# Kernel tuning notes

Measured on AMD Instinct MI355X. Metric: run time of the kernel, lower is better.

The kernel has to match this reference:

```python
import jax, jax.numpy as jnp
import numpy as np

NUM_TIMES = 1024  # times are drawn from [0, 1024), used as fixed segment count
N = 16777216


def setup_inputs() -> dict:
    key = jax.random.key(0)
    k1, k2, k3 = jax.random.split(key, 3)
    outs = jax.random.normal(k1, (N,), dtype=jnp.float32)
    T_E = jax.random.randint(k2, (N,), 0, 2, dtype=jnp.int32)
    T_T = jax.random.randint(k3, (N,), 0, NUM_TIMES, dtype=jnp.int32)
    return {"outs": outs, "T_E": T_E, "T_T": T_T}


def reference(outs, T_E, T_T):
    # E[E > 0] = 1  -> binary event indicator
    E = (T_E > 0).astype(outs.dtype)
    # Y_label_T = |T_T| ; integer times act directly as segment ids
    seg_ids = jnp.abs(T_T)
    Obs = jnp.sum(E)
    # log of running sum of hazards: log(cumsum(exp(yhat)))
    y_hat_cumsum = jnp.log(jnp.cumsum(jnp.exp(outs)))
    # original segment_max initializes accumulator at 0, so it is clipped below at 0;
    # jnp.maximum also neutralizes -inf fill for empty segments (count=0 there anyway)
    seg_max = jnp.maximum(
        jax.ops.segment_max(y_hat_cumsum, seg_ids, num_segments=NUM_TIMES), 0.0
    )
    seg_cnt = jax.ops.segment_sum(E, seg_ids, num_segments=NUM_TIMES)
    loss_s2 = jnp.sum(seg_max * seg_cnt)
    loss_s1 = jnp.sum(outs * E)
    return (loss_s2 - loss_s1) / Obs
```

## Files before the change

kernel.cpp:

```cpp
#include <hip/hip_runtime.h>

#define NUM_SEGS 1024
#define CHUNK_LOG 13
#define CHUNK (1 << CHUNK_LOG)
#define SUBCH 4
#define SUPER (CHUNK * SUBCH)
#define BLK 512
#define NWAVE (BLK / 64)
#define SEGBLK 256

__device__ __forceinline__ float waveReduceSumF(float v) {
#pragma unroll
    for (int off = 32; off > 0; off >>= 1) v += __shfl_down(v, off, 64);
    return v;
}
__device__ __forceinline__ double waveReduceSumD(double v) {
#pragma unroll
    for (int off = 32; off > 0; off >>= 1) v += __shfl_down(v, off, 64);
    return v;
}
__device__ __forceinline__ unsigned waveReduceSumU(unsigned v) {
#pragma unroll
    for (int off = 32; off > 0; off >>= 1) v += __shfl_down(v, off, 64);
    return v;
}
__device__ __forceinline__ int waveReduceMaxI(int v) {
#pragma unroll
    for (int off = 32; off > 0; off >>= 1) {
        const int o = __shfl_down(v, off, 64);
        v = o > v ? o : v;
    }
    return v;
}

__global__ void init_kernel(unsigned* __restrict__ seg_cnt,
                            float* __restrict__ csums, int nChunks,
                            unsigned* __restrict__ obs,
                            double* __restrict__ loss1,
                            double* __restrict__ loss2,
                            unsigned* __restrict__ done) {
    const int t = blockIdx.x * blockDim.x + threadIdx.x;
    if (t < NUM_SEGS) seg_cnt[t] = 0u;
    if (t < nChunks) csums[t] = 0.f;
    if (t == 0) { obs[0] = 0u; loss1[0] = 0.0; loss2[0] = 0.0; done[0] = 0u; }
}

__global__ __launch_bounds__(BLK, 4) void pass1_kernel(
    const float* __restrict__ outs, const int* __restrict__ te,
    const int* __restrict__ tt, int N, int nChunks,
    float* __restrict__ csums, unsigned* __restrict__ seg_cnt,
    unsigned* __restrict__ obs, double* __restrict__ loss1) {
    __shared__ unsigned hist[NUM_SEGS];
    __shared__ float redF[NWAVE];
    __shared__ unsigned redU[NWAVE];

    for (int t = threadIdx.x; t < NUM_SEGS; t += BLK) hist[t] = 0u;
    __syncthreads();

    const int lane = threadIdx.x & 63;
    const int wid = threadIdx.x >> 6;
    const int superBase = blockIdx.x * SUPER;

    float sE[SUBCH] = {0.f, 0.f, 0.f, 0.f};
    float sumOE = 0.f;
    unsigned cntE = 0u;

    if (superBase + SUPER <= N) {
#pragma unroll
        for (int u = 0; u < SUBCH * 4; ++u) {
            const int k = u >> 2, it = u & 3;
            const int i = superBase + (k << CHUNK_LOG) + (wid << 10) + (it << 8) +
                          (lane << 2);
            const float4 o = *reinterpret_cast<const float4*>(outs + i);
            const int4 ev = *reinterpret_cast<const int4*>(te + i);
            const int4 sv = *reinterpret_cast<const int4*>(tt + i);
            const float e0 = __expf(o.x), e1 = __expf(o.y);
            const float e2 = __expf(o.z), e3 = __expf(o.w);
            sE[k] += (e0 + e1) + (e2 + e3);
            const int s0 = sv.x < 0 ? -sv.x : sv.x;
            const int s1 = sv.y < 0 ? -sv.y : sv.y;
            const int s2 = sv.z < 0 ? -sv.z : sv.z;
            const int s3 = sv.w < 0 ? -sv.w : sv.w;
            if (ev.x > 0) { cntE++; sumOE += o.x; atomicAdd(&hist[s0], 1u); }
            if (ev.y > 0) { cntE++; sumOE += o.y; atomicAdd(&hist[s1], 1u); }
            if (ev.z > 0) { cntE++; sumOE += o.z; atomicAdd(&hist[s2], 1u); }
            if (ev.w > 0) { cntE++; sumOE += o.w; atomicAdd(&hist[s3], 1u); }
        }
    } else {
        for (int k = 0; k < SUBCH; ++k) {
            const int cbase = superBase + k * CHUNK;
            if (cbase >= N) break;
            const int end = (cbase + CHUNK < N) ? cbase + CHUNK : N;
            for (int i = cbase + (int)threadIdx.x; i < end; i += BLK) {
                const float o = outs[i];
                const int e = te[i];
                int s = tt[i]; s = s < 0 ? -s : s;
                sE[k] += __expf(o);
                if (e > 0) { cntE++; sumOE += o; atomicAdd(&hist[s], 1u); }
            }
        }
    }

#pragma unroll
    for (int k = 0; k < SUBCH; ++k) {
        const float w = waveReduceSumF(sE[k]);
        if (lane == 0) {
            const int cidx = (superBase >> CHUNK_LOG) + k;
            if (cidx < nChunks) atomicAdd(&csums[cidx], w);
        }
    }

    __syncthreads();

    for (int t = threadIdx.x; t < NUM_SEGS; t += BLK) {
        const unsigned h = hist[t];
        if (h) atomicAdd(&seg_cnt[t], h);
    }

    const float wOE = waveReduceSumF(sumOE);
    const unsigned wC = waveReduceSumU(cntE);
    if (lane == 0) { redF[wid] = wOE; redU[wid] = wC; }
    __syncthreads();
    if (threadIdx.x == 0) {
        float oe = 0.f; unsigned c = 0u;
#pragma unroll
        for (int j = 0; j < NWAVE; ++j) { oe += redF[j]; c += redU[j]; }
        atomicAdd(loss1, (double)oe);
        atomicAdd(obs, c);
    }
}

__global__ __launch_bounds__(SEGBLK) void seg_final_kernel(
    const float* __restrict__ outs, const int* __restrict__ tt,
    const float* __restrict__ csums, const unsigned* __restrict__ seg_cnt,
    const double* __restrict__ loss1, double* __restrict__ loss2,
    const unsigned* __restrict__ obs, unsigned* __restrict__ done,
    float* __restrict__ out, int N, int nChunks) {
    __shared__ double redD[SEGBLK / 64];
    __shared__ float redF[SEGBLK / 64];
    __shared__ int redI[SEGBLK / 64];
    __shared__ int s_li;

    const int t = blockIdx.x;
    const unsigned cnt = seg_cnt[t];
    const int lane = threadIdx.x & 63, wid = threadIdx.x >> 6;

    if (cnt != 0u) {
        int c = nChunks - 1;
        int LI = -1;
        for (;;) {
            const int base = c << CHUNK_LOG;
            const int end = (base + CHUNK < N) ? base + CHUNK : N;
            const int span = end - base;
            const int qspan = span & ~3;
            int li = -1;
            for (int i = base + ((int)threadIdx.x << 2); i < base + qspan;
                 i += SEGBLK * 4) {
                const int4 sv = *reinterpret_cast<const int4*>(tt + i);
                const int s0 = sv.x < 0 ? -sv.x : sv.x;
                const int s1 = sv.y < 0 ? -sv.y : sv.y;
                const int s2 = sv.z < 0 ? -sv.z : sv.z;
                const int s3 = sv.w < 0 ? -sv.w : sv.w;
                if (s3 == t) li = i + 3;
                else if (s2 == t) li = i + 2;
                else if (s1 == t) li = i + 1;
                else if (s0 == t) li = i;
            }
            for (int i = base + qspan + (int)threadIdx.x; i < end; i += SEGBLK) {
                int s = tt[i]; s = s < 0 ? -s : s;
                if (s == t && i > li) li = i;
            }
            li = waveReduceMaxI(li);
            if (lane == 0) redI[wid] = li;
            __syncthreads();
            if (threadIdx.x == 0) {
                int m = redI[0];
#pragma unroll
                for (int j = 1; j < SEGBLK / 64; ++j) m = redI[j] > m ? redI[j] : m;
                s_li = m;
            }
            __syncthreads();
            LI = s_li;
            if (LI >= 0 || --c < 0) break;
        }

        if (LI >= 0) {
            double p = 0.0;
            for (int j = threadIdx.x; j < c; j += SEGBLK) p += (double)csums[j];
            p = waveReduceSumD(p);
            if (lane == 0) redD[wid] = p;

            const int base = c << CHUNK_LOG;
            float fs = 0.f;
            for (int i = base + (int)threadIdx.x; i <= LI; i += SEGBLK)
                fs += __expf(outs[i]);
            fs = waveReduceSumF(fs);
            if (lane == 0) redF[wid] = fs;
            __syncthreads();
            if (threadIdx.x == 0) {
                double pre = 0.0;
                float fsum = 0.f;
#pragma unroll
                for (int j = 0; j < SEGBLK / 64; ++j) { pre += redD[j]; fsum += redF[j]; }
                double sm = log(pre + (double)fsum);
                if (sm < 0.0) sm = 0.0;
                atomicAdd(loss2, sm * (double)cnt);
            }
        }
    }

    if (threadIdx.x == 0) {
        __threadfence();
        const unsigned d = atomicAdd(done, 1u);
        if (d == (unsigned)(gridDim.x - 1)) {
            const double l2 = atomicAdd(loss2, 0.0);
            const double l1 = *(volatile const double*)loss1;
            const unsigned o = *(volatile const unsigned*)obs;
            out[0] = (float)((l2 - l1) / (double)o);
        }
    }
}

extern "C" void kernel_launch(void* const* d_in, const int* in_sizes, int n_in,
                              void* d_out, int out_size, void* d_ws, size_t ws_size,
                              hipStream_t stream) {
    const float* outs = (const float*)d_in[0];
    const int* te = (const int*)d_in[1];
    const int* tt = (const int*)d_in[2];
    const int N = in_sizes[0];
    float* out = (float*)d_out;

    const int nChunks = (N + CHUNK - 1) / CHUNK;

    char* ws = (char*)d_ws;
    double* d_loss1 = (double*)ws;
    double* d_loss2 = d_loss1 + 1;
    float* d_csums = (float*)(ws + 16);
    unsigned* d_segcnt = (unsigned*)(d_csums + nChunks);
    unsigned* d_obs = d_segcnt + NUM_SEGS;
    unsigned* d_done = d_obs + 1;

    const int initThreads = (nChunks > NUM_SEGS ? nChunks : NUM_SEGS);
    init_kernel<<<(initThreads + 255) / 256, 256, 0, stream>>>(
        d_segcnt, d_csums, nChunks, d_obs, d_loss1, d_loss2, d_done);
    const int nSuper = (N + SUPER - 1) / SUPER;
    pass1_kernel<<<nSuper, BLK, 0, stream>>>(outs, te, tt, N, nChunks, d_csums,
                                             d_segcnt, d_obs, d_loss1);
    seg_final_kernel<<<NUM_SEGS, SEGBLK, 0, stream>>>(
        outs, tt, d_csums, d_segcnt, d_loss1, d_loss2, d_obs, d_done, out, N,
        nChunks);
}
```

Baseline: 249.2 us.

## Batch deeper loads per thread and reduce chunk sums in shared memory

Halves block size and super-chunk size, and restructures the main loop to issue 8 float4/int4 loads per chunk up front before computing, to raise memory-level parallelism. Per-chunk exp sums are reduced across waves in shared memory and written directly by thread 0 instead of via global atomics. One block barrier is removed by moving the wave reductions before the existing sync. More blocks, each with fewer waves, change occupancy and register pressure. The tail path still uses atomics on csums, which must have been zeroed.

```diff
diff --git a/kernel.cpp b/kernel.cpp
--- a/kernel.cpp
+++ b/kernel.cpp
@@ -3,10 +3,11 @@
 #define NUM_SEGS 1024
 #define CHUNK_LOG 13
 #define CHUNK (1 << CHUNK_LOG)
-#define SUBCH 4
+#define SUBCH 2
 #define SUPER (CHUNK * SUBCH)
-#define BLK 512
+#define BLK 256
 #define NWAVE (BLK / 64)
+#define DEPTH 8
 #define SEGBLK 256
 
 __device__ __forceinline__ float waveReduceSumF(float v) {
@@ -51,6 +52,7 @@
     float* __restrict__ csums, unsigned* __restrict__ seg_cnt,
     unsigned* __restrict__ obs, double* __restrict__ loss1) {
     __shared__ unsigned hist[NUM_SEGS];
+    __shared__ float redC[SUBCH][NWAVE];
     __shared__ float redF[NWAVE];
     __shared__ unsigned redU[NWAVE];
 
@@ -61,54 +63,66 @@
     const int wid = threadIdx.x >> 6;
     const int superBase = blockIdx.x * SUPER;
 
-    float sE[SUBCH] = {0.f, 0.f, 0.f, 0.f};
     float sumOE = 0.f;
     unsigned cntE = 0u;
 
     if (superBase + SUPER <= N) {
-#pragma unroll
-        for (int u = 0; u < SUBCH * 4; ++u) {
-            const int k = u >> 2, it = u & 3;
-            const int i = superBase + (k << CHUNK_LOG) + (wid << 10) + (it << 8) +
-                          (lane << 2);
-            const float4 o = *reinterpret_cast<const float4*>(outs + i);
-            const int4 ev = *reinterpret_cast<const int4*>(te + i);
-            const int4 sv = *reinterpret_cast<const int4*>(tt + i);
-            const float e0 = __expf(o.x), e1 = __expf(o.y);
-            const float e2 = __expf(o.z), e3 = __expf(o.w);
-            sE[k] += (e0 + e1) + (e2 + e3);
-            const int s0 = sv.x < 0 ? -sv.x : sv.x;
-            const int s1 = sv.y < 0 ? -sv.y : sv.y;
-            const int s2 = sv.z < 0 ? -sv.z : sv.z;
-            const int s3 = sv.w < 0 ? -sv.w : sv.w;
-            if (ev.x > 0) { cntE++; sumOE += o.x; atomicAdd(&hist[s0], 1u); }
-            if (ev.y > 0) { cntE++; sumOE += o.y; atomicAdd(&hist[s1], 1u); }
-            if (ev.z > 0) { cntE++; sumOE += o.z; atomicAdd(&hist[s2], 1u); }
-            if (ev.w > 0) { cntE++; sumOE += o.w; atomicAdd(&hist[s3], 1u); }
+        const int i0 = superBase + ((int)threadIdx.x << 2);
+#pragma unroll
+        for (int k = 0; k < SUBCH; ++k) {
+            float4 O[DEPTH];
+            int4 E[DEPTH], S[DEPTH];
+#pragma unroll
+            for (int j = 0; j < DEPTH; ++j) {
+                const int idx = i0 + k * CHUNK + j * (BLK * 4);
+                O[j] = *reinterpret_cast<const float4*>(outs + idx);
+                E[j] = *reinterpret_cast<const int4*>(te + idx);
+                S[j] = *reinterpret_cast<const int4*>(tt + idx);
+            }
+            float s = 0.f;
+#pragma unroll
+            for (int j = 0; j < DEPTH; ++j) {
+                const float4 o = O[j];
+                const int4 ev = E[j];
+                const int4 sv = S[j];
+                s += (__expf(o.x) + __expf(o.y)) + (__expf(o.z) + __expf(o.w));
+                const int s0 = sv.x < 0 ? -sv.x : sv.x;
+                const int s1 = sv.y < 0 ? -sv.y : sv.y;
+                const int s2 = sv.z < 0 ? -sv.z : sv.z;
+                const int s3 = sv.w < 0 ? -sv.w : sv.w;
+                if (ev.x > 0) { cntE++; sumOE += o.x; atomicAdd(&hist[s0], 1u); }
+                if (ev.y > 0) { cntE++; sumOE += o.y; atomicAdd(&hist[s1], 1u); }
+                if (ev.z > 0) { cntE++; sumOE += o.z; atomicAdd(&hist[s2], 1u); }
+                if (ev.w > 0) { cntE++; sumOE += o.w; atomicAdd(&hist[s3], 1u); }
+            }
+            const float w = waveReduceSumF(s);
+            if (lane == 0) redC[k][wid] = w;
         }
     } else {
+        if (lane == 0) {
+#pragma unroll
+            for (int k = 0; k < SUBCH; ++k) redC[k][wid] = 0.f;
+        }
         for (int k = 0; k < SUBCH; ++k) {
             const int cbase = superBase + k * CHUNK;
             if (cbase >= N) break;
             const int end = (cbase + CHUNK < N) ? cbase + CHUNK : N;
+            float s = 0.f;
             for (int i = cbase + (int)threadIdx.x; i < end; i += BLK) {
                 const float o = outs[i];
                 const int e = te[i];
-                int s = tt[i]; s = s < 0 ? -s : s;
-                sE[k] += __expf(o);
-                if (e > 0) { cntE++; sumOE += o; atomicAdd(&hist[s], 1u); }
-            }
-        }
-    }
-
-#pragma unroll
-    for (int k = 0; k < SUBCH; ++k) {
-        const float w = waveReduceSumF(sE[k]);
-        if (lane == 0) {
-            const int cidx = (superBase >> CHUNK_LOG) + k;
-            if (cidx < nChunks) atomicAdd(&csums[cidx], w);
-        }
-    }
+                int sg = tt[i]; sg = sg < 0 ? -sg : sg;
+                s += __expf(o);
+                if (e > 0) { cntE++; sumOE += o; atomicAdd(&hist[sg], 1u); }
+            }
+            const float w = waveReduceSumF(s);
+            if (lane == 0 && w != 0.f) atomicAdd(&csums[cbase >> CHUNK_LOG], w);
+        }
+    }
+
+    const float wOE = waveReduceSumF(sumOE);
+    const unsigned wC = waveReduceSumU(cntE);
+    if (lane == 0) { redF[wid] = wOE; redU[wid] = wC; }
 
     __syncthreads();
 
@@ -117,11 +131,17 @@
         if (h) atomicAdd(&seg_cnt[t], h);
     }
 
-    const float wOE = waveReduceSumF(sumOE);
-    const unsigned wC = waveReduceSumU(cntE);
-    if (lane == 0) { redF[wid] = wOE; redU[wid] = wC; }
-    __syncthreads();
     if (threadIdx.x == 0) {
+        if (superBase + SUPER <= N) {
+            const int c0 = superBase >> CHUNK_LOG;
+#pragma unroll
+            for (int k = 0; k < SUBCH; ++k) {
+                float cs = 0.f;
+#pragma unroll
+                for (int j = 0; j < NWAVE; ++j) cs += redC[k][j];
+                csums[c0 + k] = cs;
+            }
+        }
         float oe = 0.f; unsigned c = 0u;
 #pragma unroll
         for (int j = 0; j < NWAVE; ++j) { oe += redF[j]; c += redU[j]; }
```

Result: no change. 244.4 us (-1.9%).
